# Kernel optimization log

Measured on AMD Instinct MI355X. Metric: run time of the kernel, lower is better.

Reference implementation:

```python
import jax, jax.numpy as jnp
import numpy as np

N = 10000   # num_nodes
E = 320000  # num_edges
D = 256     # feature / hidden dim
H = 256


def adj_lap(edge_index, n):
    """Dense normalized adjacency (gcn_norm, no self loops) and sym Laplacian."""
    row, col = edge_index[0], edge_index[1]
    # dense 0/1 adjacency (duplicate edges overwrite with same value, as in the loop)
    A = jnp.zeros((n, n), dtype=jnp.float32).at[row, col].set(1.0)
    # gcn_norm: deg = scatter(w, col) -> column sums
    deg_c = A.sum(axis=0)
    dinv_c = jnp.where(deg_c > 0, jax.lax.rsqrt(jnp.maximum(deg_c, 1e-12)), 0.0)
    anorm = dinv_c[:, None] * A * dinv_c[None, :]
    # get_laplacian 'sym': deg = scatter(w, row) -> row sums; L = I - D^-1/2 A D^-1/2
    deg_r = A.sum(axis=1)
    dinv_r = jnp.where(deg_r > 0, jax.lax.rsqrt(jnp.maximum(deg_r, 1e-12)), 0.0)
    lap = jnp.eye(n, dtype=jnp.float32) - dinv_r[:, None] * A * dinv_r[None, :]
    return lap, anorm


def gcn2(x, M, W1, b1, W2, b2):
    # pretrain_model: two-layer spectral GCN using propagation matrix M
    h = jax.nn.relu(M @ (x @ W1) + b1)
    return M @ (h @ W2) + b2


def setup_inputs() -> dict:
    key = jax.random.key(0)
    k1, k2, k3, k4 = jax.random.split(key, 4)
    x = jax.random.normal(k1, (N, D), dtype=jnp.float32)
    edge_index = jax.random.randint(k2, (2, E), 0, N, dtype=jnp.int64)
    W1 = jax.random.normal(k3, (D, H), dtype=jnp.float32) * 0.05
    b1 = jnp.zeros((H,), dtype=jnp.float32)
    W2 = jax.random.normal(k4, (H, H), dtype=jnp.float32) * 0.05
    b2 = jnp.zeros((H,), dtype=jnp.float32)
    return {"x": x, "edge_index": edge_index, "W1": W1, "b1": b1, "W2": W2, "b2": b2}


def reference(x, edge_index, W1, b1, W2, b2):
    # identity augmentor: x1 = x2 = x, edge_index1 = edge_index2 = edge_index,
    # so adj_lap is identical for both branches (computed once).
    lsym, anorm = adj_lap(edge_index, x.shape[0])
    z1 = gcn2(x, lsym, W1, b1, W2, b2)   # 'high' pass
    z2 = gcn2(x, anorm, W1, b1, W2, b2)  # 'low' pass
    z = z2
    return (z, z1, z2)
```

## Files before the change

### kernel.cpp

```cpp
#include <hip/hip_runtime.h>

#define NN 10000
#define EE 320000
#define HH 256
#define BKT 192

typedef __attribute__((ext_vector_type(8))) short bf16x8;
typedef __attribute__((ext_vector_type(4))) float f32x4;

__device__ float bf2f(unsigned int v) {
    return __uint_as_float(v << 16);
}
__device__ unsigned short f2bf(float f) {
    unsigned int i = __float_as_uint(f);
    return (unsigned short)((i + 0x7fffu + ((i >> 16) & 1u)) >> 16);
}
__device__ unsigned int fp8e(float f) {
    float a = fabsf(f);
    a = fminf(a, 448.0f);
    unsigned int bits = __float_as_uint(a * __uint_as_float(0x03800000u));
    bits = bits + 0x7ffffu + ((bits >> 20) & 1u);
    unsigned int r = bits >> 20;
    if (r > 0x7eu) r = 0x7eu;
    return r | ((__float_as_uint(f) >> 24) & 0x80u);
}
__device__ float fp8d(unsigned int b) {
    float mag = __uint_as_float((b & 0x7fu) << 20) * __uint_as_float(0x7B800000u);
    return __uint_as_float(((b & 0x80u) << 24) | __float_as_uint(mag));
}
__device__ unsigned int pk2(unsigned short a, unsigned short b) {
    return (unsigned int)a | ((unsigned int)b << 16);
}

__device__ int eload(const void* ei, int is64, int idx) {
    if (is64) return (int)(((const long long*)ei)[idx]);
    return ((const int*)ei)[idx];
}

__global__ void k_init(const unsigned int* xu, const unsigned int* eu, int* flags,
                       int* slotcnt, int* deg_c) {
    int b = blockIdx.x, t = threadIdx.x;
    int i = b * 256 + t;
    if (i < NN) { slotcnt[i] = 0; deg_c[i] = 0; }
    if (b != 0) return;
    __shared__ int odd_nz;
    __shared__ int plaus;
    if (t == 0) { odd_nz = 0; plaus = 0; }
    __syncthreads();
    if (t < 64) {
        for (int k = t; k < 256; k += 64) {
            if (eu[2 * k + 1] != 0) atomicOr(&odd_nz, 1);
        }
        unsigned int lo = xu[t] & 0xffffu;
        unsigned int ex = (lo >> 7) & 0xffu;
        if (lo == 0u || (ex >= 90u && ex <= 150u)) atomicAdd(&plaus, 1);
    }
    __syncthreads();
    if (t == 0) {
        flags[0] = odd_nz ? 0 : 1;
        flags[1] = (plaus >= 56) ? 0 : 1;
    }
}

__global__ void k_prep_scatter(const void* W1, const void* W2, const void* ei,
                               const int* flags, unsigned short* W1sw,
                               unsigned short* W2sw, int* slotcnt,
                               unsigned short* bucket) {
    int b = blockIdx.x;
    if (b >= 64) {
        int e = (b - 64) * 256 + threadIdx.x;
        int is64 = flags[0];
        int r = eload(ei, is64, e);
        int c = eload(ei, is64, EE + e);
        if (r < 0 || r >= NN || c < 0 || c >= NN) return;
        int slot = atomicAdd(&slotcnt[r], 1);
        if (slot < BKT) bucket[(size_t)r * BKT + slot] = (unsigned short)c;
        return;
    }
    const void* W = (b < 32) ? W1 : W2;
    unsigned short* O = (b < 32) ? W1sw : W2sw;
    int g = ((b < 32) ? b : b - 32) * 256 + threadIdx.x;
    int lane = g & 63;
    int n = (g >> 6) & 15;
    int ks = g >> 10;
    int coln = n * 16 + (lane & 15);
    int krow = ks * 32 + ((lane >> 4) & 3) * 8;
    unsigned short v[8];
    if (flags[1]) {
        const float* Wf = (const float*)W;
        #pragma unroll
        for (int j = 0; j < 8; j++) v[j] = f2bf(Wf[(size_t)(krow + j) * HH + coln]);
    } else {
        const unsigned short* Wh = (const unsigned short*)W;
        #pragma unroll
        for (int j = 0; j < 8; j++) v[j] = Wh[(size_t)(krow + j) * HH + coln];
    }
    uint4 p;
    p.x = pk2(v[0], v[1]); p.y = pk2(v[2], v[3]);
    p.z = pk2(v[4], v[5]); p.w = pk2(v[6], v[7]);
    *(uint4*)(O + (size_t)g * 8) = p;
}

__global__ void k_gy_dedup(const void* A, const unsigned short* Bsw,
                           unsigned char* Yf8, void* Oout, const int* flags,
                           const int* slotcnt, unsigned short* bucket,
                           int* deg_r, int* deg_c) {
    __shared__ unsigned short As[16][264];
    __shared__ int lds[4][BKT];
    __shared__ int cnt[4];
    int b = blockIdx.x;
    int tid = threadIdx.x;
    if (b < 625) {
        int r0 = b * 16;
        int af32 = flags[1];
        {
            int row = tid >> 4, seg = tid & 15;
            if (af32) {
                const float* ap = (const float*)A + (size_t)(r0 + row) * HH + seg * 16;
                unsigned short v[16];
                #pragma unroll
                for (int j = 0; j < 16; j += 4) {
                    float4 q = *(const float4*)(ap + j);
                    v[j] = f2bf(q.x); v[j + 1] = f2bf(q.y);
                    v[j + 2] = f2bf(q.z); v[j + 3] = f2bf(q.w);
                }
                uint4 p0, p1;
                p0.x = pk2(v[0], v[1]);  p0.y = pk2(v[2], v[3]);
                p0.z = pk2(v[4], v[5]);  p0.w = pk2(v[6], v[7]);
                p1.x = pk2(v[8], v[9]);  p1.y = pk2(v[10], v[11]);
                p1.z = pk2(v[12], v[13]); p1.w = pk2(v[14], v[15]);
                *(uint4*)&As[row][seg * 16] = p0;
                *(uint4*)&As[row][seg * 16 + 8] = p1;
            } else {
                const unsigned short* ap = (const unsigned short*)A + (size_t)(r0 + row) * HH + seg * 16;
                *(uint4*)&As[row][seg * 16] = *(const uint4*)ap;
                *(uint4*)&As[row][seg * 16 + 8] = *(const uint4*)(ap + 8);
            }
        }
        __syncthreads();
        int wv = tid >> 6;
        int lane = tid & 63;
        int quad = lane >> 4;
        int l16 = lane & 15;
        f32x4 acc[4] = {{0,0,0,0},{0,0,0,0},{0,0,0,0},{0,0,0,0}};
        for (int ks = 0; ks < 8; ks++) {
            bf16x8 af = *(const bf16x8*)&As[l16][ks * 32 + quad * 8];
            #pragma unroll
            for (int t = 0; t < 4; t++) {
                int n = wv * 4 + t;
                bf16x8 bf = *(const bf16x8*)(Bsw + ((size_t)(ks * 16 + n) * 64 + lane) * 8);
                acc[t] = __builtin_amdgcn_mfma_f32_16x16x32_bf16(af, bf, acc[t], 0, 0, 0);
            }
        }
        size_t chunkW = (size_t)NN * HH;
        #pragma unroll
        for (int t = 0; t < 4; t++) {
            int cn = (wv * 4 + t) * 16 + l16;
            #pragma unroll
            for (int r = 0; r < 4; r++) {
                int row = r0 + quad * 4 + r;
                float v = acc[t][r];
                size_t idx = (size_t)row * HH + cn;
                Yf8[idx] = (unsigned char)fp8e(v);
                if (af32) ((float*)Oout)[2 * chunkW + idx] = v;
                else      ((unsigned short*)Oout)[2 * chunkW + idx] = f2bf(v);
            }
        }
        return;
    }
    int wave = tid >> 6;
    int lane = tid & 63;
    int i = (b - 625) * 4 + wave;
    int d = slotcnt[i];
    if (d > BKT) d = BKT;
    if (lane == 0) cnt[wave] = 0;
    unsigned short* bp = bucket + (size_t)i * BKT;
    for (int t = lane; t < d; t += 64) lds[wave][t] = (int)bp[t];
    __syncthreads();
    for (int t = lane; t < d; t += 64) {
        int c = lds[wave][t];
        int dup = 0;
        for (int u = 0; u < t; u++) dup |= (lds[wave][u] == c);
        if (!dup) {
            int p = atomicAdd(&cnt[wave], 1);
            bp[p] = (unsigned short)c;
            atomicAdd(&deg_c[c], 1);
        }
    }
    __syncthreads();
    if (lane == 0) deg_r[i] = cnt[wave];
}

__global__ void k_dinv2(const int* deg_r, const int* deg_c, float* dinv2) {
    int i = blockIdx.x * 256 + threadIdx.x;
    if (i >= NN) return;
    int dr = deg_r[i], dc = deg_c[i];
    dinv2[2 * i]     = dr > 0 ? rsqrtf((float)dr) : 0.0f;
    dinv2[2 * i + 1] = dc > 0 ? rsqrtf((float)dc) : 0.0f;
}

__global__ void k_spmm_mid(const unsigned char* Yf8, const void* Oout,
                           const unsigned short* bucket, const int* ucnt,
                           const float* dinv2, const void* bias,
                           const int* flags, unsigned short* H1, unsigned short* H2) {
    int wave = threadIdx.x >> 6;
    int lane = threadIdx.x & 63;
    int fb = lane * 4;
    int i = blockIdx.x * 4 + wave;
    float a1[4] = {0, 0, 0, 0};
    float a2[4] = {0, 0, 0, 0};
    int n = ucnt[i];
    const unsigned short* cp = bucket + (size_t)i * BKT;
    int t = 0;
    for (; t + 4 <= n; t += 4) {
        ushort4 c4 = *(const ushort4*)(cp + t);
        int cx[4] = {(int)c4.x, (int)c4.y, (int)c4.z, (int)c4.w};
        float2 w[4];
        #pragma unroll
        for (int j = 0; j < 4; j++) w[j] = *(const float2*)(dinv2 + 2 * cx[j]);
        unsigned int gv[4];
        #pragma unroll
        for (int j = 0; j < 4; j++)
            gv[j] = *(const unsigned int*)(Yf8 + (size_t)cx[j] * 256 + fb);
        #pragma unroll
        for (int j = 0; j < 4; j++) {
            #pragma unroll
            for (int k = 0; k < 4; k++) {
                float y = fp8d((gv[j] >> (8 * k)) & 0xffu);
                a1[k] += w[j].x * y;
                a2[k] += w[j].y * y;
            }
        }
    }
    for (; t < n; t++) {
        int c = (int)cp[t];
        float2 w = *(const float2*)(dinv2 + 2 * c);
        unsigned int g = *(const unsigned int*)(Yf8 + (size_t)c * 256 + fb);
        #pragma unroll
        for (int k = 0; k < 4; k++) {
            float y = fp8d((g >> (8 * k)) & 0xffu);
            a1[k] += w.x * y;
            a2[k] += w.y * y;
        }
    }
    int f32io = flags[1];
    float bv[4];
    if (f32io) {
        const float* bp = (const float*)bias + fb;
        #pragma unroll
        for (int k = 0; k < 4; k++) bv[k] = bp[k];
    } else {
        uint2 br = *(const uint2*)((const unsigned short*)bias + fb);
        bv[0] = bf2f(br.x & 0xffffu); bv[1] = bf2f(br.x >> 16);
        bv[2] = bf2f(br.y & 0xffffu); bv[3] = bf2f(br.y >> 16);
    }
    float2 wii = *(const float2*)(dinv2 + 2 * i);
    size_t chunkW = (size_t)NN * HH;
    float yv[4];
    if (f32io) {
        const float* sp = (const float*)Oout + 2 * chunkW + (size_t)i * HH + fb;
        #pragma unroll
        for (int k = 0; k < 4; k++) yv[k] = sp[k];
    } else {
        uint2 yi = *(const uint2*)((const unsigned short*)Oout + 2 * chunkW + (size_t)i * HH + fb);
        yv[0] = bf2f(yi.x & 0xffffu); yv[1] = bf2f(yi.x >> 16);
        yv[2] = bf2f(yi.y & 0xffffu); yv[3] = bf2f(yi.y >> 16);
    }
    float h1[4], h2[4];
    #pragma unroll
    for (int k = 0; k < 4; k++) {
        h1[k] = fmaxf(0.f, yv[k] - wii.x * a1[k] + bv[k]);
        h2[k] = fmaxf(0.f, wii.y * a2[k] + bv[k]);
    }
    uint2 p1, p2;
    p1.x = pk2(f2bf(h1[0]), f2bf(h1[1])); p1.y = pk2(f2bf(h1[2]), f2bf(h1[3]));
    p2.x = pk2(f2bf(h2[0]), f2bf(h2[1])); p2.y = pk2(f2bf(h2[2]), f2bf(h2[3]));
    *(uint2*)(H1 + (size_t)i * HH + fb) = p1;
    *(uint2*)(H2 + (size_t)i * HH + fb) = p2;
}

__global__ void k_gg(const unsigned short* H1, const unsigned short* H2,
                     const unsigned short* Bsw, unsigned char* G12f8,
                     void* Oout, const int* flags) {
    __shared__ unsigned short As[16][264];
    int b = blockIdx.x;
    int tid = threadIdx.x;
    int isG1 = (b < 625);
    const unsigned short* A = isG1 ? H1 : H2;
    int r0 = (isG1 ? b : b - 625) * 16;
    {
        int row = tid >> 4, seg = tid & 15;
        const unsigned short* ap = A + (size_t)(r0 + row) * HH + seg * 16;
        *(uint4*)&As[row][seg * 16] = *(const uint4*)ap;
        *(uint4*)&As[row][seg * 16 + 8] = *(const uint4*)(ap + 8);
    }
    __syncthreads();
    int wv = tid >> 6;
    int lane = tid & 63;
    int quad = lane >> 4;
    int l16 = lane & 15;
    f32x4 acc[4] = {{0,0,0,0},{0,0,0,0},{0,0,0,0},{0,0,0,0}};
    for (int ks = 0; ks < 8; ks++) {
        bf16x8 af = *(const bf16x8*)&As[l16][ks * 32 + quad * 8];
        #pragma unroll
        for (int t = 0; t < 4; t++) {
            int n = wv * 4 + t;
            bf16x8 bf = *(const bf16x8*)(Bsw + ((size_t)(ks * 16 + n) * 64 + lane) * 8);
            acc[t] = __builtin_amdgcn_mfma_f32_16x16x32_bf16(af, bf, acc[t], 0, 0, 0);
        }
    }
    size_t chunkW = (size_t)NN * HH;
    int f32io = flags[1];
    #pragma unroll
    for (int t = 0; t < 4; t++) {
        int cn = (wv * 4 + t) * 16 + l16;
        #pragma unroll
        for (int r = 0; r < 4; r++) {
            int row = r0 + quad * 4 + r;
            float v = acc[t][r];
            if (isG1) {
                G12f8[(size_t)row * 512 + cn] = (unsigned char)fp8e(v);
                size_t idx = (size_t)row * HH + cn;
                if (f32io) ((float*)Oout)[chunkW + idx] = v;
                else       ((unsigned short*)Oout)[chunkW + idx] = f2bf(v);
            } else {
                G12f8[(size_t)row * 512 + 256 + cn] = (unsigned char)fp8e(v);
            }
        }
    }
}

__global__ void k_spmm_fin(const unsigned char* G12f8, const unsigned short* bucket,
                           const int* ucnt, const float* dinv2, const void* bias,
                           const int* flags, void* Oout) {
    int wave = threadIdx.x >> 6;
    int lane = threadIdx.x & 63;
    int half = lane >> 5;
    int sub = lane & 31;
    int fb = sub * 8;
    int goff = half * 256 + fb;
    int i = blockIdx.x * 4 + wave;
    float acc[8] = {0, 0, 0, 0, 0, 0, 0, 0};
    int n = ucnt[i];
    const unsigned short* cp = bucket + (size_t)i * BKT;
    int t = 0;
    for (; t + 4 <= n; t += 4) {
        ushort4 c4 = *(const ushort4*)(cp + t);
        int cx[4] = {(int)c4.x, (int)c4.y, (int)c4.z, (int)c4.w};
        float ws[4];
        #pragma unroll
        for (int j = 0; j < 4; j++) {
            float2 w = *(const float2*)(dinv2 + 2 * cx[j]);
            ws[j] = half ? w.y : w.x;
        }
        uint2 gv[4];
        #pragma unroll
        for (int j = 0; j < 4; j++)
            gv[j] = *(const uint2*)(G12f8 + (size_t)cx[j] * 512 + goff);
        #pragma unroll
        for (int j = 0; j < 4; j++) {
            #pragma unroll
            for (int k = 0; k < 4; k++) {
                float y = fp8d((gv[j].x >> (8 * k)) & 0xffu);
                acc[k] += ws[j] * y;
            }
            #pragma unroll
            for (int k = 0; k < 4; k++) {
                float y = fp8d((gv[j].y >> (8 * k)) & 0xffu);
                acc[4 + k] += ws[j] * y;
            }
        }
    }
    for (; t < n; t++) {
        int c = (int)cp[t];
        float2 w = *(const float2*)(dinv2 + 2 * c);
        float wsel = half ? w.y : w.x;
        uint2 g = *(const uint2*)(G12f8 + (size_t)c * 512 + goff);
        #pragma unroll
        for (int k = 0; k < 4; k++) acc[k] += wsel * fp8d((g.x >> (8 * k)) & 0xffu);
        #pragma unroll
        for (int k = 0; k < 4; k++) acc[4 + k] += wsel * fp8d((g.y >> (8 * k)) & 0xffu);
    }
    int f32io = flags[1];
    float bv[8];
    if (f32io) {
        const float* bp = (const float*)bias + fb;
        #pragma unroll
        for (int k = 0; k < 8; k++) bv[k] = bp[k];
    } else {
        uint4 br = *(const uint4*)((const unsigned short*)bias + fb);
        bv[0] = bf2f(br.x & 0xffffu); bv[1] = bf2f(br.x >> 16);
        bv[2] = bf2f(br.y & 0xffffu); bv[3] = bf2f(br.y >> 16);
        bv[4] = bf2f(br.z & 0xffffu); bv[5] = bf2f(br.z >> 16);
        bv[6] = bf2f(br.w & 0xffffu); bv[7] = bf2f(br.w >> 16);
    }
    float2 wii = *(const float2*)(dinv2 + 2 * i);
    size_t base = (size_t)i * HH + fb;
    size_t chunkW = (size_t)NN * HH;
    float z[8];
    if (half == 0) {
        float gvv[8];
        if (f32io) {
            const float* sp = (const float*)Oout + chunkW + base;
            #pragma unroll
            for (int k = 0; k < 8; k++) gvv[k] = sp[k];
        } else {
            uint4 gi = *(const uint4*)((const unsigned short*)Oout + chunkW + base);
            gvv[0] = bf2f(gi.x & 0xffffu); gvv[1] = bf2f(gi.x >> 16);
            gvv[2] = bf2f(gi.y & 0xffffu); gvv[3] = bf2f(gi.y >> 16);
            gvv[4] = bf2f(gi.z & 0xffffu); gvv[5] = bf2f(gi.z >> 16);
            gvv[6] = bf2f(gi.w & 0xffffu); gvv[7] = bf2f(gi.w >> 16);
        }
        #pragma unroll
        for (int k = 0; k < 8; k++) z[k] = gvv[k] - wii.x * acc[k] + bv[k];
        if (f32io) {
            float* o = (float*)Oout + chunkW + base;
            *(float4*)o = make_float4(z[0], z[1], z[2], z[3]);
            *(float4*)(o + 4) = make_float4(z[4], z[5], z[6], z[7]);
        } else {
            uint4 p;
            p.x = pk2(f2bf(z[0]), f2bf(z[1])); p.y = pk2(f2bf(z[2]), f2bf(z[3]));
            p.z = pk2(f2bf(z[4]), f2bf(z[5])); p.w = pk2(f2bf(z[6]), f2bf(z[7]));
            *(uint4*)((unsigned short*)Oout + chunkW + base) = p;
        }
    } else {
        #pragma unroll
        for (int k = 0; k < 8; k++) z[k] = wii.y * acc[k] + bv[k];
        if (f32io) {
            float* o0 = (float*)Oout + base;
            float* o2 = (float*)Oout + 2 * chunkW + base;
            float4 pa = make_float4(z[0], z[1], z[2], z[3]);
            float4 pb = make_float4(z[4], z[5], z[6], z[7]);
            *(float4*)o0 = pa; *(float4*)(o0 + 4) = pb;
            *(float4*)o2 = pa; *(float4*)(o2 + 4) = pb;
        } else {
            uint4 p;
            p.x = pk2(f2bf(z[0]), f2bf(z[1])); p.y = pk2(f2bf(z[2]), f2bf(z[3]));
            p.z = pk2(f2bf(z[4]), f2bf(z[5])); p.w = pk2(f2bf(z[6]), f2bf(z[7]));
            *(uint4*)((unsigned short*)Oout + base) = p;
            *(uint4*)((unsigned short*)Oout + 2 * chunkW + base) = p;
        }
    }
}

extern "C" void kernel_launch(void* const* d_in, const int* in_sizes, int n_in,
                              void* d_out, int out_size, void* d_ws, size_t ws_size,
                              hipStream_t stream) {
    const void* x = 0; const void* ei = 0;
    const void* W1 = 0; const void* b1 = 0; const void* W2 = 0; const void* b2 = 0;
    for (int i = 0; i < n_in; i++) {
        int s = in_sizes[i];
        if (s == NN * HH) x = d_in[i];
        else if (s == 2 * EE) ei = d_in[i];
        else if (s == HH * HH) { if (!W1) W1 = d_in[i]; else W2 = d_in[i]; }
        else if (s == HH) { if (!b1) b1 = d_in[i]; else b2 = d_in[i]; }
    }

    char* ws = (char*)d_ws;
    size_t off = 0;
    int* flags = (int*)(ws + off); off += 256;
    int* slotcnt = (int*)(ws + off); off += (size_t)NN * 4;
    int* deg_c = (int*)(ws + off); off += (size_t)NN * 4;
    int* deg_r = (int*)(ws + off); off += (size_t)NN * 4;
    float* dinv2 = (float*)(ws + off); off += (size_t)NN * 8;
    unsigned short* bucket = (unsigned short*)(ws + off); off += (size_t)NN * BKT * 2;
    unsigned short* W1sw = (unsigned short*)(ws + off); off += (size_t)HH * HH * 2;
    unsigned short* W2sw = (unsigned short*)(ws + off); off += (size_t)HH * HH * 2;
    unsigned char* Yf8 = (unsigned char*)(ws + off); off += (size_t)NN * 256;
    unsigned char* G12f8 = (unsigned char*)(ws + off); off += (size_t)NN * 512;
    unsigned short* H1 = (unsigned short*)(ws + off); off += (size_t)NN * HH * 2;
    unsigned short* H2 = (unsigned short*)(ws + off); off += (size_t)NN * HH * 2;

    k_init<<<40, 256, 0, stream>>>((const unsigned int*)x, (const unsigned int*)ei,
                                   flags, slotcnt, deg_c);
    k_prep_scatter<<<64 + EE / 256, 256, 0, stream>>>(W1, W2, ei, flags, W1sw, W2sw,
                                                      slotcnt, bucket);
    k_gy_dedup<<<625 + NN / 4, 256, 0, stream>>>(x, W1sw, Yf8, d_out, flags,
                                                 slotcnt, bucket, deg_r, deg_c);
    k_dinv2<<<(NN + 255) / 256, 256, 0, stream>>>(deg_r, deg_c, dinv2);
    k_spmm_mid<<<NN / 4, 256, 0, stream>>>(Yf8, d_out, bucket, deg_r, dinv2, b1,
                                           flags, H1, H2);
    k_gg<<<1250, 256, 0, stream>>>(H1, H2, W2sw, G12f8, d_out, flags);
    k_spmm_fin<<<NN / 4, 256, 0, stream>>>(G12f8, bucket, deg_r, dinv2, b2, flags, d_out);
}
```

Baseline: 203.3 us.

## Deduplicate edges with a global bitmap and merge launches into five kernels

Edge deduplication now uses a 100M-bit global bitmap with atomicOr, so only first-seen edges are written to buckets and counted. This replaces the per-row quadratic LDS dedup pass and the separate degree/dinv kernel; degrees are packed as int pairs and rsqrt is recomputed on the fly in the SpMM kernels. The init, weight swizzle and flag detection are merged into one launch, and the scatter is fused with the first GEMM. The cost is zeroing a 12.5MB bitmap (aliased onto the G12f8 buffer) and issuing extra global atomics per edge.

```diff
diff --git a/kernel.cpp b/kernel.cpp
--- a/kernel.cpp
+++ b/kernel.cpp
@@ -4,6 +4,7 @@
 #define EE 320000
 #define HH 256
 #define BKT 192
+#define ZU4 786370
 
 typedef __attribute__((ext_vector_type(8))) short bf16x8;
 typedef __attribute__((ext_vector_type(4))) float f32x4;
@@ -31,193 +32,188 @@
 __device__ unsigned int pk2(unsigned short a, unsigned short b) {
     return (unsigned int)a | ((unsigned int)b << 16);
 }
-
 __device__ int eload(const void* ei, int is64, int idx) {
     if (is64) return (int)(((const long long*)ei)[idx]);
     return ((const int*)ei)[idx];
 }
-
-__global__ void k_init(const unsigned int* xu, const unsigned int* eu, int* flags,
-                       int* slotcnt, int* deg_c) {
+__device__ __forceinline__ float dinv_of(int d) {
+    return d > 0 ? rsqrtf((float)d) : 0.0f;
+}
+
+__global__ void k_A(const void* x, const void* ei, const void* W1, const void* W2,
+                    int* flags, int* cnt2, unsigned int* bitmap,
+                    unsigned short* W1sw, unsigned short* W2sw) {
     int b = blockIdx.x, t = threadIdx.x;
-    int i = b * 256 + t;
-    if (i < NN) { slotcnt[i] = 0; deg_c[i] = 0; }
-    if (b != 0) return;
-    __shared__ int odd_nz;
+    if (b >= 65) {
+        int base = (b - 65) * 1024 + t;
+        uint4 z = make_uint4(0, 0, 0, 0);
+        #pragma unroll
+        for (int j = 0; j < 4; j++) {
+            int idx = base + j * 256;
+            if (idx < 5120) ((uint4*)cnt2)[idx] = z;
+            else if (idx < ZU4) ((uint4*)bitmap)[idx - 5120] = z;
+        }
+        return;
+    }
+    if (b == 0) {
+        __shared__ int s0, s1;
+        if (t == 0) { s0 = 0; s1 = 0; }
+        __syncthreads();
+        if (t < 64) {
+            const unsigned int* eu = (const unsigned int*)ei;
+            const unsigned int* xu = (const unsigned int*)x;
+            for (int k = t; k < 256; k += 64)
+                if (eu[2 * k + 1] != 0) atomicOr(&s0, 1);
+            unsigned int lo = xu[t] & 0xffffu;
+            unsigned int ex = (lo >> 7) & 0xffu;
+            if (lo == 0u || (ex >= 90u && ex <= 150u)) atomicAdd(&s1, 1);
+        }
+        __syncthreads();
+        if (t == 0) {
+            flags[0] = s0 ? 0 : 1;
+            flags[1] = (s1 >= 56) ? 0 : 1;
+        }
+        return;
+    }
     __shared__ int plaus;
-    if (t == 0) { odd_nz = 0; plaus = 0; }
+    if (t == 0) plaus = 0;
     __syncthreads();
     if (t < 64) {
-        for (int k = t; k < 256; k += 64) {
-            if (eu[2 * k + 1] != 0) atomicOr(&odd_nz, 1);
-        }
-        unsigned int lo = xu[t] & 0xffffu;
+        unsigned int lo = ((const unsigned int*)x)[t] & 0xffffu;
         unsigned int ex = (lo >> 7) & 0xffu;
         if (lo == 0u || (ex >= 90u && ex <= 150u)) atomicAdd(&plaus, 1);
     }
     __syncthreads();
-    if (t == 0) {
-        flags[0] = odd_nz ? 0 : 1;
-        flags[1] = (plaus >= 56) ? 0 : 1;
-    }
-}
-
-__global__ void k_prep_scatter(const void* W1, const void* W2, const void* ei,
-                               const int* flags, unsigned short* W1sw,
-                               unsigned short* W2sw, int* slotcnt,
-                               unsigned short* bucket) {
+    int f32io = (plaus >= 56) ? 0 : 1;
+    int vb = b - 1;
+    const void* W = (vb < 32) ? W1 : W2;
+    unsigned short* O = (vb < 32) ? W1sw : W2sw;
+    int g = ((vb < 32) ? vb : vb - 32) * 256 + t;
+    int gl = g & 63;
+    int n = (g >> 6) & 15;
+    int ks = g >> 10;
+    int coln = n * 16 + (gl & 15);
+    int krow = ks * 32 + ((gl >> 4) & 3) * 8;
+    unsigned short v[8];
+    if (f32io) {
+        const float* Wf = (const float*)W;
+        #pragma unroll
+        for (int j = 0; j < 8; j++) v[j] = f2bf(Wf[(size_t)(krow + j) * HH + coln]);
+    } else {
+        const unsigned short* Wh = (const unsigned short*)W;
+        #pragma unroll
+        for (int j = 0; j < 8; j++) v[j] = Wh[(size_t)(krow + j) * HH + coln];
+    }
+    uint4 p;
+    p.x = pk2(v[0], v[1]); p.y = pk2(v[2], v[3]);
+    p.z = pk2(v[4], v[5]); p.w = pk2(v[6], v[7]);
+    *(uint4*)(O + (size_t)g * 8) = p;
+}
+
+__global__ void k_B(const void* x, const void* ei, const unsigned short* W1sw,
+                    const int* flags, int* cnt2, unsigned int* bitmap,
+                    unsigned short* bucket, unsigned char* Yf8, void* Oout) {
     int b = blockIdx.x;
-    if (b >= 64) {
-        int e = (b - 64) * 256 + threadIdx.x;
+    int tid = threadIdx.x;
+    if (b >= 625) {
+        int e = (b - 625) * 256 + tid;
+        if (e >= EE) return;
         int is64 = flags[0];
         int r = eload(ei, is64, e);
         int c = eload(ei, is64, EE + e);
         if (r < 0 || r >= NN || c < 0 || c >= NN) return;
-        int slot = atomicAdd(&slotcnt[r], 1);
-        if (slot < BKT) bucket[(size_t)r * BKT + slot] = (unsigned short)c;
+        unsigned int bi = (unsigned int)r * 10000u + (unsigned int)c;
+        unsigned int m = 1u << (bi & 31u);
+        unsigned int old = atomicOr(&bitmap[bi >> 5], m);
+        if (!(old & m)) {
+            int slot = atomicAdd(&cnt2[2 * r], 1);
+            if (slot < BKT) bucket[(size_t)r * BKT + slot] = (unsigned short)c;
+            atomicAdd(&cnt2[2 * c + 1], 1);
+        }
         return;
     }
-    const void* W = (b < 32) ? W1 : W2;
-    unsigned short* O = (b < 32) ? W1sw : W2sw;
-    int g = ((b < 32) ? b : b - 32) * 256 + threadIdx.x;
-    int lane = g & 63;
-    int n = (g >> 6) & 15;
-    int ks = g >> 10;
-    int coln = n * 16 + (lane & 15);
-    int krow = ks * 32 + ((lane >> 4) & 3) * 8;
-    unsigned short v[8];
-    if (flags[1]) {
-        const float* Wf = (const float*)W;
-        #pragma unroll
-        for (int j = 0; j < 8; j++) v[j] = f2bf(Wf[(size_t)(krow + j) * HH + coln]);
-    } else {
-        const unsigned short* Wh = (const unsigned short*)W;
-        #pragma unroll
-        for (int j = 0; j < 8; j++) v[j] = Wh[(size_t)(krow + j) * HH + coln];
-    }
-    uint4 p;
-    p.x = pk2(v[0], v[1]); p.y = pk2(v[2], v[3]);
-    p.z = pk2(v[4], v[5]); p.w = pk2(v[6], v[7]);
-    *(uint4*)(O + (size_t)g * 8) = p;
-}
-
-__global__ void k_gy_dedup(const void* A, const unsigned short* Bsw,
-                           unsigned char* Yf8, void* Oout, const int* flags,
-                           const int* slotcnt, unsigned short* bucket,
-                           int* deg_r, int* deg_c) {
     __shared__ unsigned short As[16][264];
-    __shared__ int lds[4][BKT];
-    __shared__ int cnt[4];
-    int b = blockIdx.x;
-    int tid = threadIdx.x;
-    if (b < 625) {
-        int r0 = b * 16;
-        int af32 = flags[1];
-        {
-            int row = tid >> 4, seg = tid & 15;
-            if (af32) {
-                const float* ap = (const float*)A + (size_t)(r0 + row) * HH + seg * 16;
-                unsigned short v[16];
-                #pragma unroll
-                for (int j = 0; j < 16; j += 4) {
-                    float4 q = *(const float4*)(ap + j);
-                    v[j] = f2bf(q.x); v[j + 1] = f2bf(q.y);
-                    v[j + 2] = f2bf(q.z); v[j + 3] = f2bf(q.w);
-                }
-                uint4 p0, p1;
-                p0.x = pk2(v[0], v[1]);  p0.y = pk2(v[2], v[3]);
-                p0.z = pk2(v[4], v[5]);  p0.w = pk2(v[6], v[7]);
-                p1.x = pk2(v[8], v[9]);  p1.y = pk2(v[10], v[11]);
-                p1.z = pk2(v[12], v[13]); p1.w = pk2(v[14], v[15]);
-                *(uint4*)&As[row][seg * 16] = p0;
-                *(uint4*)&As[row][seg * 16 + 8] = p1;
-            } else {
-                const unsigned short* ap = (const unsigned short*)A + (size_t)(r0 + row) * HH + seg * 16;
-                *(uint4*)&As[row][seg * 16] = *(const uint4*)ap;
-                *(uint4*)&As[row][seg * 16 + 8] = *(const uint4*)(ap + 8);
+    int r0 = b * 16;
+    int af32 = flags[1];
+    {
+        int row = tid >> 4, seg = tid & 15;
+        if (af32) {
+            const float* ap = (const float*)x + (size_t)(r0 + row) * HH + seg * 16;
+            unsigned short v[16];
+            #pragma unroll
+            for (int j = 0; j < 16; j += 4) {
+                float4 q = *(const float4*)(ap + j);
+                v[j] = f2bf(q.x); v[j + 1] = f2bf(q.y);
+                v[j + 2] = f2bf(q.z); v[j + 3] = f2bf(q.w);
             }
-        }
-        __syncthreads();
-        int wv = tid >> 6;
-        int lane = tid & 63;
-        int quad = lane >> 4;
-        int l16 = lane & 15;
-        f32x4 acc[4] = {{0,0,0,0},{0,0,0,0},{0,0,0,0},{0,0,0,0}};
-        for (int ks = 0; ks < 8; ks++) {
-            bf16x8 af = *(const bf16x8*)&As[l16][ks * 32 + quad * 8];
-            #pragma unroll
-            for (int t = 0; t < 4; t++) {
-                int n = wv * 4 + t;
-                bf16x8 bf = *(const bf16x8*)(Bsw + ((size_t)(ks * 16 + n) * 64 + lane) * 8);
-                acc[t] = __builtin_amdgcn_mfma_f32_16x16x32_bf16(af, bf, acc[t], 0, 0, 0);
-            }
-        }
-        size_t chunkW = (size_t)NN * HH;
+            uint4 p0, p1;
+            p0.x = pk2(v[0], v[1]);   p0.y = pk2(v[2], v[3]);
+            p0.z = pk2(v[4], v[5]);   p0.w = pk2(v[6], v[7]);
+            p1.x = pk2(v[8], v[9]);   p1.y = pk2(v[10], v[11]);
+            p1.z = pk2(v[12], v[13]); p1.w = pk2(v[14], v[15]);
+            *(uint4*)&As[row][seg * 16] = p0;
+            *(uint4*)&As[row][seg * 16 + 8] = p1;
+        } else {
+            const unsigned short* ap = (const unsigned short*)x + (size_t)(r0 + row) * HH + seg * 16;
+            *(uint4*)&As[row][seg * 16] = *(const uint4*)ap;
+            *(uint4*)&As[row][seg * 16 + 8] = *(const uint4*)(ap + 8);
+        }
+    }
+    __syncthreads();
+    int wv = tid >> 6;
+    int lane = tid & 63;
+    int quad = lane >> 4;
+    int l16 = lane & 15;
+    f32x4 acc[4] = {{0,0,0,0},{0,0,0,0},{0,0,0,0},{0,0,0,0}};
+    for (int ks = 0; ks < 8; ks++) {
+        bf16x8 af = *(const bf16x8*)&As[l16][ks * 32 + quad * 8];
         #pragma unroll
         for (int t = 0; t < 4; t++) {
-            int cn = (wv * 4 + t) * 16 + l16;
-            #pragma unroll
-            for (int r = 0; r < 4; r++) {
-                int row = r0 + quad * 4 + r;
-                float v = acc[t][r];
-                size_t idx = (size_t)row * HH + cn;
-                Yf8[idx] = (unsigned char)fp8e(v);
-                if (af32) ((float*)Oout)[2 * chunkW + idx] = v;
-                else      ((unsigned short*)Oout)[2 * chunkW + idx] = f2bf(v);
-            }
-        }
-        return;
-    }
-    int wave = tid >> 6;
-    int lane = tid & 63;
-    int i = (b - 625) * 4 + wave;
-    int d = slotcnt[i];
-    if (d > BKT) d = BKT;
-    if (lane == 0) cnt[wave] = 0;
-    unsigned short* bp = bucket + (size_t)i * BKT;
-    for (int t = lane; t < d; t += 64) lds[wave][t] = (int)bp[t];
-    __syncthreads();
-    for (int t = lane; t < d; t += 64) {
-        int c = lds[wave][t];
-        int dup = 0;
-        for (int u = 0; u < t; u++) dup |= (lds[wave][u] == c);
-        if (!dup) {
-            int p = atomicAdd(&cnt[wave], 1);
-            bp[p] = (unsigned short)c;
-            atomicAdd(&deg_c[c], 1);
-        }
-    }
-    __syncthreads();
-    if (lane == 0) deg_r[i] = cnt[wave];
-}
-
-__global__ void k_dinv2(const int* deg_r, const int* deg_c, float* dinv2) {
-    int i = blockIdx.x * 256 + threadIdx.x;
-    if (i >= NN) return;
-    int dr = deg_r[i], dc = deg_c[i];
-    dinv2[2 * i]     = dr > 0 ? rsqrtf((float)dr) : 0.0f;
-    dinv2[2 * i + 1] = dc > 0 ? rsqrtf((float)dc) : 0.0f;
-}
-
-__global__ void k_spmm_mid(const unsigned char* Yf8, const void* Oout,
-                           const unsigned short* bucket, const int* ucnt,
-                           const float* dinv2, const void* bias,
-                           const int* flags, unsigned short* H1, unsigned short* H2) {
+            int n = wv * 4 + t;
+            bf16x8 bf = *(const bf16x8*)(W1sw + ((size_t)(ks * 16 + n) * 64 + lane) * 8);
+            acc[t] = __builtin_amdgcn_mfma_f32_16x16x32_bf16(af, bf, acc[t], 0, 0, 0);
+        }
+    }
+    size_t chunkW = (size_t)NN * HH;
+    #pragma unroll
+    for (int t = 0; t < 4; t++) {
+        int cn = (wv * 4 + t) * 16 + l16;
+        #pragma unroll
+        for (int r = 0; r < 4; r++) {
+            int row = r0 + quad * 4 + r;
+            float vv = acc[t][r];
+            size_t idx = (size_t)row * HH + cn;
+            Yf8[idx] = (unsigned char)fp8e(vv);
+            if (af32) ((float*)Oout)[2 * chunkW + idx] = vv;
+            else      ((unsigned short*)Oout)[2 * chunkW + idx] = f2bf(vv);
+        }
+    }
+}
+
+__global__ void k_C(const unsigned char* Yf8, const void* Oout,
+                    const unsigned short* bucket, const int* cnt2,
+                    const void* bias, const int* flags,
+                    unsigned short* H1, unsigned short* H2) {
     int wave = threadIdx.x >> 6;
     int lane = threadIdx.x & 63;
     int fb = lane * 4;
     int i = blockIdx.x * 4 + wave;
     float a1[4] = {0, 0, 0, 0};
     float a2[4] = {0, 0, 0, 0};
-    int n = ucnt[i];
+    int2 ddi = *(const int2*)(cnt2 + 2 * i);
+    int n = ddi.x;
     const unsigned short* cp = bucket + (size_t)i * BKT;
     int t = 0;
     for (; t + 4 <= n; t += 4) {
         ushort4 c4 = *(const ushort4*)(cp + t);
         int cx[4] = {(int)c4.x, (int)c4.y, (int)c4.z, (int)c4.w};
-        float2 w[4];
-        #pragma unroll
-        for (int j = 0; j < 4; j++) w[j] = *(const float2*)(dinv2 + 2 * cx[j]);
+        float wx[4], wy[4];
+        #pragma unroll
+        for (int j = 0; j < 4; j++) {
+            int2 dd = *(const int2*)(cnt2 + 2 * cx[j]);
+            wx[j] = dinv_of(dd.x);
+            wy[j] = dinv_of(dd.y);
+        }
         unsigned int gv[4];
         #pragma unroll
         for (int j = 0; j < 4; j++)
@@ -227,20 +223,22 @@
             #pragma unroll
             for (int k = 0; k < 4; k++) {
                 float y = fp8d((gv[j] >> (8 * k)) & 0xffu);
-                a1[k] += w[j].x * y;
-                a2[k] += w[j].y * y;
+                a1[k] += wx[j] * y;
+                a2[k] += wy[j] * y;
             }
         }
     }
     for (; t < n; t++) {
         int c = (int)cp[t];
-        float2 w = *(const float2*)(dinv2 + 2 * c);
+        int2 dd = *(const int2*)(cnt2 + 2 * c);
+        float wx = dinv_of(dd.x);
+        float wy = dinv_of(dd.y);
         unsigned int g = *(const unsigned int*)(Yf8 + (size_t)c * 256 + fb);
         #pragma unroll
         for (int k = 0; k < 4; k++) {
             float y = fp8d((g >> (8 * k)) & 0xffu);
-            a1[k] += w.x * y;
-            a2[k] += w.y * y;
+            a1[k] += wx * y;
+            a2[k] += wy * y;
         }
     }
     int f32io = flags[1];
@@ -254,7 +252,8 @@
         bv[0] = bf2f(br.x & 0xffffu); bv[1] = bf2f(br.x >> 16);
         bv[2] = bf2f(br.y & 0xffffu); bv[3] = bf2f(br.y >> 16);
     }
-    float2 wii = *(const float2*)(dinv2 + 2 * i);
+    float wiix = dinv_of(ddi.x);
+    float wiiy = dinv_of(ddi.y);
     size_t chunkW = (size_t)NN * HH;
     float yv[4];
     if (f32io) {
@@ -269,8 +268,8 @@
     float h1[4], h2[4];
     #pragma unroll
     for (int k = 0; k < 4; k++) {
-        h1[k] = fmaxf(0.f, yv[k] - wii.x * a1[k] + bv[k]);
-        h2[k] = fmaxf(0.f, wii.y * a2[k] + bv[k]);
+        h1[k] = fmaxf(0.f, yv[k] - wiix * a1[k] + bv[k]);
+        h2[k] = fmaxf(0.f, wiiy * a2[k] + bv[k]);
     }
     uint2 p1, p2;
     p1.x = pk2(f2bf(h1[0]), f2bf(h1[1])); p1.y = pk2(f2bf(h1[2]), f2bf(h1[3]));
@@ -279,9 +278,9 @@
     *(uint2*)(H2 + (size_t)i * HH + fb) = p2;
 }
 
-__global__ void k_gg(const unsigned short* H1, const unsigned short* H2,
-                     const unsigned short* Bsw, unsigned char* G12f8,
-                     void* Oout, const int* flags) {
+__global__ void k_D(const unsigned short* H1, const unsigned short* H2,
+                    const unsigned short* Bsw, unsigned char* G12f8,
+                    void* Oout, const int* flags) {
     __shared__ unsigned short As[16][264];
     int b = blockIdx.x;
     int tid = threadIdx.x;
@@ -317,22 +316,22 @@
         #pragma unroll
         for (int r = 0; r < 4; r++) {
             int row = r0 + quad * 4 + r;
-            float v = acc[t][r];
+            float vv = acc[t][r];
             if (isG1) {
-                G12f8[(size_t)row * 512 + cn] = (unsigned char)fp8e(v);
+                G12f8[(size_t)row * 512 + cn] = (unsigned char)fp8e(vv);
                 size_t idx = (size_t)row * HH + cn;
-                if (f32io) ((float*)Oout)[chunkW + idx] = v;
-                else       ((unsigned short*)Oout)[chunkW + idx] = f2bf(v);
+                if (f32io) ((float*)Oout)[chunkW + idx] = vv;
+                else       ((unsigned short*)Oout)[chunkW + idx] = f2bf(vv);
             } else {
-                G12f8[(size_t)row * 512 + 256 + cn] = (unsigned char)fp8e(v);
+                G12f8[(size_t)row * 512 + 256 + cn] = (unsigned char)fp8e(vv);
             }
         }
     }
 }
 
-__global__ void k_spmm_fin(const unsigned char* G12f8, const unsigned short* bucket,
-                           const int* ucnt, const float* dinv2, const void* bias,
-                           const int* flags, void* Oout) {
+__global__ void k_E(const unsigned char* G12f8, const unsigned short* bucket,
+                    const int* cnt2, const void* bias, const int* flags,
+                    void* Oout) {
     int wave = threadIdx.x >> 6;
     int lane = threadIdx.x & 63;
     int half = lane >> 5;
@@ -341,7 +340,8 @@
     int goff = half * 256 + fb;
     int i = blockIdx.x * 4 + wave;
     float acc[8] = {0, 0, 0, 0, 0, 0, 0, 0};
-    int n = ucnt[i];
+    int2 ddi = *(const int2*)(cnt2 + 2 * i);
+    int n = ddi.x;
     const unsigned short* cp = bucket + (size_t)i * BKT;
     int t = 0;
     for (; t + 4 <= n; t += 4) {
@@ -350,8 +350,8 @@
         float ws[4];
         #pragma unroll
         for (int j = 0; j < 4; j++) {
-            float2 w = *(const float2*)(dinv2 + 2 * cx[j]);
-            ws[j] = half ? w.y : w.x;
+            int2 dd = *(const int2*)(cnt2 + 2 * cx[j]);
+            ws[j] = dinv_of(half ? dd.y : dd.x);
         }
         uint2 gv[4];
         #pragma unroll
@@ -373,8 +373,8 @@
     }
     for (; t < n; t++) {
         int c = (int)cp[t];
-        float2 w = *(const float2*)(dinv2 + 2 * c);
-        float wsel = half ? w.y : w.x;
+        int2 dd = *(const int2*)(cnt2 + 2 * c);
+        float wsel = dinv_of(half ? dd.y : dd.x);
         uint2 g = *(const uint2*)(G12f8 + (size_t)c * 512 + goff);
         #pragma unroll
         for (int k = 0; k < 4; k++) acc[k] += wsel * fp8d((g.x >> (8 * k)) & 0xffu);
@@ -394,11 +394,11 @@
         bv[4] = bf2f(br.z & 0xffffu); bv[5] = bf2f(br.z >> 16);
         bv[6] = bf2f(br.w & 0xffffu); bv[7] = bf2f(br.w >> 16);
     }
-    float2 wii = *(const float2*)(dinv2 + 2 * i);
     size_t base = (size_t)i * HH + fb;
     size_t chunkW = (size_t)NN * HH;
     float z[8];
     if (half == 0) {
+        float wiix = dinv_of(ddi.x);
         float gvv[8];
         if (f32io) {
             const float* sp = (const float*)Oout + chunkW + base;
@@ -412,7 +412,7 @@
             gvv[6] = bf2f(gi.w & 0xffffu); gvv[7] = bf2f(gi.w >> 16);
         }
         #pragma unroll
-        for (int k = 0; k < 8; k++) z[k] = gvv[k] - wii.x * acc[k] + bv[k];
+        for (int k = 0; k < 8; k++) z[k] = gvv[k] - wiix * acc[k] + bv[k];
         if (f32io) {
             float* o = (float*)Oout + chunkW + base;
             *(float4*)o = make_float4(z[0], z[1], z[2], z[3]);
@@ -424,8 +424,9 @@
             *(uint4*)((unsigned short*)Oout + chunkW + base) = p;
         }
     } else {
-        #pragma unroll
-        for (int k = 0; k < 8; k++) z[k] = wii.y * acc[k] + bv[k];
+        float wiiy = dinv_of(ddi.y);
+        #pragma unroll
+        for (int k = 0; k < 8; k++) z[k] = wiiy * acc[k] + bv[k];
         if (f32io) {
             float* o0 = (float*)Oout + base;
             float* o2 = (float*)Oout + 2 * chunkW + base;
@@ -459,10 +460,7 @@
     char* ws = (char*)d_ws;
     size_t off = 0;
     int* flags = (int*)(ws + off); off += 256;
-    int* slotcnt = (int*)(ws + off); off += (size_t)NN * 4;
-    int* deg_c = (int*)(ws + off); off += (size_t)NN * 4;
-    int* deg_r = (int*)(ws + off); off += (size_t)NN * 4;
-    float* dinv2 = (float*)(ws + off); off += (size_t)NN * 8;
+    int* cnt2 = (int*)(ws + off); off += 81920;
     unsigned short* bucket = (unsigned short*)(ws + off); off += (size_t)NN * BKT * 2;
     unsigned short* W1sw = (unsigned short*)(ws + off); off += (size_t)HH * HH * 2;
     unsigned short* W2sw = (unsigned short*)(ws + off); off += (size_t)HH * HH * 2;
@@ -470,16 +468,11 @@
     unsigned char* G12f8 = (unsigned char*)(ws + off); off += (size_t)NN * 512;
     unsigned short* H1 = (unsigned short*)(ws + off); off += (size_t)NN * HH * 2;
     unsigned short* H2 = (unsigned short*)(ws + off); off += (size_t)NN * HH * 2;
-
-    k_init<<<40, 256, 0, stream>>>((const unsigned int*)x, (const unsigned int*)ei,
-                                   flags, slotcnt, deg_c);
-    k_prep_scatter<<<64 + EE / 256, 256, 0, stream>>>(W1, W2, ei, flags, W1sw, W2sw,
-                                                      slotcnt, bucket);
-    k_gy_dedup<<<625 + NN / 4, 256, 0, stream>>>(x, W1sw, Yf8, d_out, flags,
-                                                 slotcnt, bucket, deg_r, deg_c);
-    k_dinv2<<<(NN + 255) / 256, 256, 0, stream>>>(deg_r, deg_c, dinv2);
-    k_spmm_mid<<<NN / 4, 256, 0, stream>>>(Yf8, d_out, bucket, deg_r, dinv2, b1,
-                                           flags, H1, H2);
-    k_gg<<<1250, 256, 0, stream>>>(H1, H2, W2sw, G12f8, d_out, flags);
-    k_spmm_fin<<<NN / 4, 256, 0, stream>>>(G12f8, bucket, deg_r, dinv2, b2, flags, d_out);
-}
+    unsigned int* bitmap = (unsigned int*)G12f8;
+
+    k_A<<<833, 256, 0, stream>>>(x, ei, W1, W2, flags, cnt2, bitmap, W1sw, W2sw);
+    k_B<<<1875, 256, 0, stream>>>(x, ei, W1sw, flags, cnt2, bitmap, bucket, Yf8, d_out);
+    k_C<<<NN / 4, 256, 0, stream>>>(Yf8, d_out, bucket, cnt2, b1, flags, H1, H2);
+    k_D<<<1250, 256, 0, stream>>>(H1, H2, W2sw, G12f8, d_out, flags);
+    k_E<<<NN / 4, 256, 0, stream>>>(G12f8, bucket, cnt2, b2, flags, d_out);
+}
```

After: 215.1 us. 1.06x slower.
